# Kernel optimization log

Measured on AMD Instinct MI355X. Metric: run time of the kernel, lower is better.

The kernel has to match this reference:

```python
import jax, jax.numpy as jnp
import numpy as np

DIM = 1024
N_HEADS = 16
HEAD_DIM = DIM // N_HEADS
SCALE = HEAD_DIM ** -0.5


def setup_inputs() -> dict:
    key = jax.random.key(0)
    k1, k2, k3 = jax.random.split(key, 3)
    x = jax.random.normal(k1, (4, 2048, DIM), dtype=jnp.float32)
    w_qkv = jax.random.normal(k2, (DIM, 3 * DIM), dtype=jnp.float32) * (DIM ** -0.5)
    w_proj = jax.random.normal(k3, (DIM, DIM), dtype=jnp.float32) * (DIM ** -0.5)
    b_proj = jnp.zeros((DIM,), dtype=jnp.float32)
    return {"x": x, "w_qkv": w_qkv, "w_proj": w_proj, "b_proj": b_proj}


def reference(x, w_qkv, w_proj, b_proj):
    b, s, d = x.shape
    # qkv projection (no bias), split into q, k, v with per-head layout
    qkv = (x @ w_qkv).reshape(b, s, 3, N_HEADS, HEAD_DIM)
    q, k, v = jnp.moveaxis(qkv, 2, 0)  # each [b, s, h, hd]
    # scaled dot-product attention
    scores = jnp.einsum('bqhd,bkhd->bhqk', q, k) * SCALE
    attn = jax.nn.softmax(scores, axis=-1)
    out = jnp.einsum('bhqk,bkhd->bqhd', attn, v).reshape(b, s, d)
    # output projection (with bias)
    return out @ w_proj + b_proj
```

## Files before the change

kernel.cpp:

```cpp
#include <hip/hip_runtime.h>

#define DIM 1024
#define NHEADS 16
#define HD 64
#define SEQ 2048
#define BATCH 4
#define MROWS (BATCH * SEQ)
#define N3 (3 * DIM)
#define SCALE 0.125f
#define LOG2E 1.4426950408889634f
#define SM_C (SCALE * LOG2E)
#define SMAX 16.0f

typedef __attribute__((ext_vector_type(8))) __bf16 bf16x8;
typedef __attribute__((ext_vector_type(4))) __bf16 bf16x4;
typedef __attribute__((ext_vector_type(4))) float f32x4;

#define MFMA16(a, b, c) __builtin_amdgcn_mfma_f32_16x16x32_bf16((a), (b), (c), 0, 0, 0)

#define GLDS16(g, l)                                                        \
  __builtin_amdgcn_global_load_lds(                                         \
      (const __attribute__((address_space(1))) void*)(g),                   \
      (__attribute__((address_space(3))) void*)(l), 16, 0, 0)

__device__ __forceinline__ unsigned short f2bf(float f) {
  union { float f; unsigned u; } v;
  v.f = f;
  unsigned r = v.u + 0x7fffu + ((v.u >> 16) & 1u);
  return (unsigned short)(r >> 16);
}

__device__ __forceinline__ float exp2_hw(float x) {
  float r;
  asm("v_exp_f32 %0, %1" : "=v"(r) : "v"(x));
  return r;
}


__device__ __forceinline__ void tcast_tile(const float* __restrict__ in,
                                           unsigned short* __restrict__ out,
                                           int K, int N, int bx, int by,
                                           int t) {
  __shared__ float tile[32][33];
  int c = t & 31, r8 = t >> 5;
  int n0 = bx * 32, k0 = by * 32;
#pragma unroll
  for (int i = 0; i < 4; ++i) {
    int kr = r8 + i * 8;
    tile[kr][c] = in[(size_t)(k0 + kr) * N + n0 + c];
  }
  __syncthreads();
#pragma unroll
  for (int i = 0; i < 4; ++i) {
    int nr = r8 + i * 8;
    out[(size_t)(n0 + nr) * K + k0 + c] = f2bf(tile[c][nr]);
  }
}

__global__ void prep_kernel(const float* __restrict__ x,
                            unsigned short* __restrict__ xb,
                            const float* __restrict__ wqkv,
                            unsigned short* __restrict__ wqkvT,
                            const float* __restrict__ wproj,
                            unsigned short* __restrict__ wprojT) {
  const int bid = blockIdx.x, t = threadIdx.x;
  if (bid < 8192) {
    int i = bid * 256 + t;
    float4 v = ((const float4*)x)[i];
    ushort4 o;
    o.x = f2bf(v.x); o.y = f2bf(v.y); o.z = f2bf(v.z); o.w = f2bf(v.w);
    ((ushort4*)xb)[i] = o;
  } else if (bid < 11264) {
    int local = bid - 8192;
    tcast_tile(wqkv, wqkvT, DIM, N3, local % 96, local / 96, t);
  } else {
    int local = bid - 11264;
    tcast_tile(wproj, wprojT, DIM, DIM, local % 32, local / 32, t);
  }
}


__global__ __launch_bounds__(256, 3)
void gemm_qkv_kernel(const unsigned short* __restrict__ A,
                     const unsigned short* __restrict__ Bt,
                     unsigned short* __restrict__ Qb,
                     unsigned short* __restrict__ Kb,
                     unsigned short* __restrict__ Vt) {
  __shared__ __align__(16) unsigned short As[128 * 64];
  __shared__ __align__(16) unsigned short Bs[128 * 64];
  int t = threadIdx.x;
  int w = t >> 6, l = t & 63;
  int lane16 = l & 15, lhi = l >> 4;
  int mbase = blockIdx.y * 128, nbase = blockIdx.x * 128;
  int wm = (w >> 1) * 64, wn = (w & 1) * 64;

  const int srow = t >> 3;
  const int sslot = (t & 7) ^ ((t >> 3) & 7);
  const unsigned short* Ag = A + (size_t)(mbase + srow) * 1024 + sslot * 8;
  const unsigned short* Bg = Bt + (size_t)(nbase + srow) * 1024 + sslot * 8;

  const int sl0 = ((lhi ^ (lane16 & 7)) << 4);
  const char* Ard = (const char*)As + (wm + lane16) * 128;
  const char* Brd = (const char*)Bs + (wn + lane16) * 128;

  f32x4 acc[4][4];
  f32x4 z4 = {0.f, 0.f, 0.f, 0.f};
#pragma unroll
  for (int i = 0; i < 4; ++i)
#pragma unroll
    for (int j = 0; j < 4; ++j) acc[i][j] = z4;

  for (int kt = 0; kt < 1024; kt += 64) {
#pragma unroll
    for (int i = 0; i < 4; ++i) {
      GLDS16(Ag + (size_t)(i * 32) * 1024 + kt, (char*)As + i * 4096 + w * 1024);
      GLDS16(Bg + (size_t)(i * 32) * 1024 + kt, (char*)Bs + i * 4096 + w * 1024);
    }
    __syncthreads();
#pragma unroll
    for (int kh = 0; kh < 2; ++kh) {
      const int so = sl0 ^ (kh << 6);
      bf16x8 af[4], bfr[4];
#pragma unroll
      for (int mi = 0; mi < 4; ++mi)
        af[mi] = *(const bf16x8*)(Ard + mi * 2048 + so);
#pragma unroll
      for (int ni = 0; ni < 4; ++ni)
        bfr[ni] = *(const bf16x8*)(Brd + ni * 2048 + so);
#pragma unroll
      for (int mi = 0; mi < 4; ++mi)
#pragma unroll
        for (int ni = 0; ni < 4; ++ni)
          acc[mi][ni] = MFMA16(af[mi], bfr[ni], acc[mi][ni]);
    }
    __syncthreads();
  }

#pragma unroll
  for (int mi = 0; mi < 4; ++mi) {
#pragma unroll
    for (int ni = 0; ni < 4; ++ni) {
#pragma unroll
      for (int r = 0; r < 4; ++r) {
        int grow = mbase + wm + mi * 16 + (lhi << 2) + r;
        int gcol = nbase + wn + ni * 16 + lane16;
        int b = grow >> 11, s = grow & 2047;
        unsigned short val = f2bf(acc[mi][ni][r]);
        if (gcol < 1024) {
          int h = gcol >> 6, d = gcol & 63;
          Qb[((size_t)(b * 16 + h) * 2048 + s) * 64 + d] = val;
        } else if (gcol < 2048) {
          int n2 = gcol - 1024;
          int h = n2 >> 6, d = n2 & 63;
          Kb[((size_t)(b * 16 + h) * 2048 + s) * 64 + d] = val;
        } else {
          int n2 = gcol - 2048;
          int h = n2 >> 6, d = n2 & 63;
          Vt[((size_t)(b * 16 + h) * 64 + d) * 2048 + s] = val;
        }
      }
    }
  }
}


__global__ __launch_bounds__(512, 4)
void attn_kernel(const unsigned short* __restrict__ Qb,
                 const unsigned short* __restrict__ Kb,
                 const unsigned short* __restrict__ Vt,
                 unsigned short* __restrict__ attn) {
  __shared__ __align__(16) unsigned short Ks[2][4096];
  __shared__ __align__(16) unsigned short Vs[2][4096];
  __shared__ __align__(16) unsigned short Ps[8][32][72];

  const int t = threadIdx.x, wv = t >> 6, l = t & 63;
  const int lane16 = l & 15, lhi = l >> 4;

  const int bid = blockIdx.x;
  const int nid = (bid & 7) * 64 + (bid >> 3);
  const int qg = nid & 7, h = (nid >> 3) & 15, b = nid >> 7;

  const unsigned short* Qp = Qb + (size_t)(b * NHEADS + h) * SEQ * HD;
  const unsigned short* Kp = Kb + (size_t)(b * NHEADS + h) * SEQ * HD;
  const unsigned short* Vp = Vt + (size_t)(b * NHEADS + h) * HD * SEQ;

  const int q0 = qg * 256 + wv * 32;

  bf16x8 qa[2][2];
#pragma unroll
  for (int mi = 0; mi < 2; ++mi)
#pragma unroll
    for (int kh = 0; kh < 2; ++kh)
      qa[mi][kh] = *(const bf16x8*)(Qp + (size_t)(q0 + mi * 16 + lane16) * HD +
                                    kh * 32 + lhi * 8);

  const int srow = t >> 3;
  const unsigned short* kg = Kp + srow * HD + (((t & 7) ^ ((t >> 5) & 7)) * 8);
  const unsigned short* vg =
      Vp + (size_t)srow * SEQ + (((t & 7) ^ ((t >> 3) & 7)) * 8);

  const int key = lane16 & 7;
  const int off0 = (lhi ^ key) << 4;
  const int off1 = off0 ^ 64;
  const char* krd = (const char*)&Ks[0][0] + lane16 * 512;
  const char* vrd = (const char*)&Vs[0][0] + lane16 * 128;
  unsigned short* pwr = &Ps[wv][0][lane16 * 4];
  const unsigned short* prd = &Ps[wv][lane16][lhi * 8];

  f32x4 z4 = {0.f, 0.f, 0.f, 0.f};
  f32x4 o[2][4];
  float lsum[2][4];
#pragma unroll
  for (int mi = 0; mi < 2; ++mi)
#pragma unroll
    for (int nd = 0; nd < 4; ++nd) o[mi][nd] = z4;
#pragma unroll
  for (int mi = 0; mi < 2; ++mi)
#pragma unroll
    for (int r = 0; r < 4; ++r) lsum[mi][r] = 0.f;

  GLDS16(kg, (char*)&Ks[0][0] + wv * 1024);
  GLDS16(vg, (char*)&Vs[0][0] + wv * 1024);
  __syncthreads();

  int cur = 0;
  for (int ti = 0; ti < SEQ / 64; ++ti) {
    if (ti < SEQ / 64 - 1) {
      const int kb = (ti + 1) * 64;
      GLDS16(kg + (size_t)kb * HD, (char*)&Ks[cur ^ 1][0] + wv * 1024);
      GLDS16(vg + kb, (char*)&Vs[cur ^ 1][0] + wv * 1024);
    }

    const char* kp = krd + cur * 8192;
    bf16x8 kf[4][2];
#pragma unroll
    for (int ni = 0; ni < 4; ++ni) {
      kf[ni][0] = *(const bf16x8*)(kp + ni * 128 + off0);
      kf[ni][1] = *(const bf16x8*)(kp + ni * 128 + off1);
    }
#pragma unroll
    for (int mi = 0; mi < 2; ++mi) {
      f32x4 s[4];
      __builtin_amdgcn_s_setprio(1);
#pragma unroll
      for (int ni = 0; ni < 4; ++ni) {
        f32x4 a = MFMA16(qa[mi][0], kf[ni][0], z4);
        s[ni] = MFMA16(qa[mi][1], kf[ni][1], a);
      }
      __builtin_amdgcn_s_setprio(0);
#pragma unroll
      for (int r = 0; r < 4; ++r) {
        float p0 = exp2_hw(__builtin_fmaf(s[0][r], SM_C, -SMAX));
        float p1 = exp2_hw(__builtin_fmaf(s[1][r], SM_C, -SMAX));
        float p2 = exp2_hw(__builtin_fmaf(s[2][r], SM_C, -SMAX));
        float p3 = exp2_hw(__builtin_fmaf(s[3][r], SM_C, -SMAX));
        lsum[mi][r] += (p0 + p1) + (p2 + p3);
        bf16x4 pk;
        pk[0] = (__bf16)p0; pk[1] = (__bf16)p1;
        pk[2] = (__bf16)p2; pk[3] = (__bf16)p3;
        *(bf16x4*)(pwr + (mi * 16 + (lhi << 2) + r) * 72) = pk;
      }
    }

    bf16x8 pa[2][2];
#pragma unroll
    for (int mi = 0; mi < 2; ++mi)
#pragma unroll
      for (int kvh = 0; kvh < 2; ++kvh)
        pa[mi][kvh] = *(const bf16x8*)(prd + mi * 16 * 72 + kvh * 32);
    const char* vp2 = vrd + cur * 8192;
    __builtin_amdgcn_s_setprio(1);
#pragma unroll
    for (int nd = 0; nd < 4; ++nd) {
      bf16x8 v0 = *(const bf16x8*)(vp2 + nd * 2048 + off0);
      bf16x8 v1 = *(const bf16x8*)(vp2 + nd * 2048 + off1);
#pragma unroll
      for (int mi = 0; mi < 2; ++mi) {
        o[mi][nd] = MFMA16(pa[mi][0], v0, o[mi][nd]);
        o[mi][nd] = MFMA16(pa[mi][1], v1, o[mi][nd]);
      }
    }
    __builtin_amdgcn_s_setprio(0);
    __syncthreads();
    cur ^= 1;
  }

#pragma unroll
  for (int mi = 0; mi < 2; ++mi)
#pragma unroll
    for (int r = 0; r < 4; ++r) {
      float ls = lsum[mi][r];
      ls += __shfl_xor(ls, 1);
      ls += __shfl_xor(ls, 2);
      ls += __shfl_xor(ls, 4);
      ls += __shfl_xor(ls, 8);
      lsum[mi][r] = 1.0f / ls;
    }
  size_t orow_base = (size_t)b * SEQ;
#pragma unroll
  for (int mi = 0; mi < 2; ++mi)
#pragma unroll
    for (int nd = 0; nd < 4; ++nd)
#pragma unroll
      for (int r = 0; r < 4; ++r) {
        int row = q0 + mi * 16 + (lhi << 2) + r;
        attn[(orow_base + row) * DIM + h * HD + nd * 16 + lane16] =
            f2bf(o[mi][nd][r] * lsum[mi][r]);
      }
}


__global__ __launch_bounds__(256, 3)
void gemm_proj_kernel(const unsigned short* __restrict__ A,
                      const unsigned short* __restrict__ Bt,
                      const float* __restrict__ bias,
                      float* __restrict__ out) {
  __shared__ __align__(16) unsigned short Asp[128 * 64];
  __shared__ __align__(16) unsigned short Bsp[128 * 64];
  int t = threadIdx.x;
  int w = t >> 6, l = t & 63;
  int lane16 = l & 15, lhi = l >> 4;
  int mbase = blockIdx.y * 128, nbase = blockIdx.x * 128;
  int wm = (w >> 1) * 64, wn = (w & 1) * 64;

  const int srow = t >> 3;
  const int sslot = (t & 7) ^ ((t >> 3) & 7);
  const unsigned short* Ag = A + (size_t)(mbase + srow) * 1024 + sslot * 8;
  const unsigned short* Bg = Bt + (size_t)(nbase + srow) * 1024 + sslot * 8;

  const int sl0 = ((lhi ^ (lane16 & 7)) << 4);
  const char* Ard = (const char*)Asp + (wm + lane16) * 128;
  const char* Brd = (const char*)Bsp + (wn + lane16) * 128;

  f32x4 acc[4][4];
  f32x4 z4 = {0.f, 0.f, 0.f, 0.f};
#pragma unroll
  for (int i = 0; i < 4; ++i)
#pragma unroll
    for (int j = 0; j < 4; ++j) acc[i][j] = z4;

  for (int kt = 0; kt < 1024; kt += 64) {
#pragma unroll
    for (int i = 0; i < 4; ++i) {
      GLDS16(Ag + (size_t)(i * 32) * 1024 + kt, (char*)Asp + i * 4096 + w * 1024);
      GLDS16(Bg + (size_t)(i * 32) * 1024 + kt, (char*)Bsp + i * 4096 + w * 1024);
    }
    __syncthreads();
#pragma unroll
    for (int kh = 0; kh < 2; ++kh) {
      const int so = sl0 ^ (kh << 6);
      bf16x8 af[4], bfr[4];
#pragma unroll
      for (int mi = 0; mi < 4; ++mi)
        af[mi] = *(const bf16x8*)(Ard + mi * 2048 + so);
#pragma unroll
      for (int ni = 0; ni < 4; ++ni)
        bfr[ni] = *(const bf16x8*)(Brd + ni * 2048 + so);
#pragma unroll
      for (int mi = 0; mi < 4; ++mi)
#pragma unroll
        for (int ni = 0; ni < 4; ++ni)
          acc[mi][ni] = MFMA16(af[mi], bfr[ni], acc[mi][ni]);
    }
    __syncthreads();
  }

#pragma unroll
  for (int mi = 0; mi < 4; ++mi) {
#pragma unroll
    for (int ni = 0; ni < 4; ++ni) {
#pragma unroll
      for (int r = 0; r < 4; ++r) {
        int grow = mbase + wm + mi * 16 + (lhi << 2) + r;
        int gcol = nbase + wn + ni * 16 + lane16;
        out[(size_t)grow * 1024 + gcol] = acc[mi][ni][r] + bias[gcol];
      }
    }
  }
}


extern "C" void kernel_launch(void* const* d_in, const int* in_sizes, int n_in,
                              void* d_out, int out_size, void* d_ws,
                              size_t ws_size, hipStream_t stream) {
  const float* x = (const float*)d_in[0];
  const float* w_qkv = (const float*)d_in[1];
  const float* w_proj = (const float*)d_in[2];
  const float* b_proj = (const float*)d_in[3];
  float* out = (float*)d_out;
  char* ws = (char*)d_ws;

  unsigned short* xb = (unsigned short*)(ws);
  unsigned short* attnb = (unsigned short*)(ws);
  unsigned short* wqkvT = (unsigned short*)(ws + (16ull << 20));
  unsigned short* wprojT = (unsigned short*)(ws + (22ull << 20));
  unsigned short* Qb = (unsigned short*)(ws + (24ull << 20));
  unsigned short* Kb = (unsigned short*)(ws + (40ull << 20));
  unsigned short* Vt = (unsigned short*)(ws + (56ull << 20));

  prep_kernel<<<12288, 256, 0, stream>>>(x, xb, w_qkv, wqkvT, w_proj, wprojT);
  gemm_qkv_kernel<<<dim3(N3 / 128, MROWS / 128), 256, 0, stream>>>(xb, wqkvT, Qb, Kb, Vt);
  attn_kernel<<<512, 512, 0, stream>>>(Qb, Kb, Vt, attnb);
  gemm_proj_kernel<<<dim3(DIM / 128, MROWS / 128), 256, 0, stream>>>(attnb, wprojT, b_proj, out);
}
```

Baseline: 206.5 us.

## Load K and V fragments directly from global memory, dropping LDS staging

```diff
diff --git a/kernel.cpp b/kernel.cpp
--- a/kernel.cpp
+++ b/kernel.cpp
@@ -169,8 +169,6 @@
                  const unsigned short* __restrict__ Kb,
                  const unsigned short* __restrict__ Vt,
                  unsigned short* __restrict__ attn) {
-  __shared__ __align__(16) unsigned short Ks[2][4096];
-  __shared__ __align__(16) unsigned short Vs[2][4096];
   __shared__ __align__(16) unsigned short Ps[8][32][72];
 
   const int t = threadIdx.x, wv = t >> 6, l = t & 63;
@@ -194,16 +192,9 @@
       qa[mi][kh] = *(const bf16x8*)(Qp + (size_t)(q0 + mi * 16 + lane16) * HD +
                                     kh * 32 + lhi * 8);
 
-  const int srow = t >> 3;
-  const unsigned short* kg = Kp + srow * HD + (((t & 7) ^ ((t >> 5) & 7)) * 8);
-  const unsigned short* vg =
-      Vp + (size_t)srow * SEQ + (((t & 7) ^ ((t >> 3) & 7)) * 8);
-
-  const int key = lane16 & 7;
-  const int off0 = (lhi ^ key) << 4;
-  const int off1 = off0 ^ 64;
-  const char* krd = (const char*)&Ks[0][0] + lane16 * 512;
-  const char* vrd = (const char*)&Vs[0][0] + lane16 * 128;
+  const unsigned short* kfb = Kp + (size_t)(4 * lane16) * HD + lhi * 8;
+  const unsigned short* vfb = Vp + (size_t)lane16 * SEQ + lhi * 8;
+
   unsigned short* pwr = &Ps[wv][0][lane16 * 4];
   const unsigned short* prd = &Ps[wv][lane16][lhi * 8];
 
@@ -219,35 +210,23 @@
 #pragma unroll
     for (int r = 0; r < 4; ++r) lsum[mi][r] = 0.f;
 
-  GLDS16(kg, (char*)&Ks[0][0] + wv * 1024);
-  GLDS16(vg, (char*)&Vs[0][0] + wv * 1024);
-  __syncthreads();
-
-  int cur = 0;
-  for (int ti = 0; ti < SEQ / 64; ++ti) {
-    if (ti < SEQ / 64 - 1) {
-      const int kb = (ti + 1) * 64;
-      GLDS16(kg + (size_t)kb * HD, (char*)&Ks[cur ^ 1][0] + wv * 1024);
-      GLDS16(vg + kb, (char*)&Vs[cur ^ 1][0] + wv * 1024);
-    }
-
-    const char* kp = krd + cur * 8192;
+  for (int kb = 0; kb < SEQ; kb += 64) {
     bf16x8 kf[4][2];
 #pragma unroll
     for (int ni = 0; ni < 4; ++ni) {
-      kf[ni][0] = *(const bf16x8*)(kp + ni * 128 + off0);
-      kf[ni][1] = *(const bf16x8*)(kp + ni * 128 + off1);
-    }
+      const unsigned short* kr = kfb + (size_t)(kb + ni) * HD;
+      kf[ni][0] = *(const bf16x8*)(kr);
+      kf[ni][1] = *(const bf16x8*)(kr + 32);
+    }
+
 #pragma unroll
     for (int mi = 0; mi < 2; ++mi) {
       f32x4 s[4];
-      __builtin_amdgcn_s_setprio(1);
 #pragma unroll
       for (int ni = 0; ni < 4; ++ni) {
         f32x4 a = MFMA16(qa[mi][0], kf[ni][0], z4);
         s[ni] = MFMA16(qa[mi][1], kf[ni][1], a);
       }
-      __builtin_amdgcn_s_setprio(0);
 #pragma unroll
       for (int r = 0; r < 4; ++r) {
         float p0 = exp2_hw(__builtin_fmaf(s[0][r], SM_C, -SMAX));
@@ -268,21 +247,17 @@
 #pragma unroll
       for (int kvh = 0; kvh < 2; ++kvh)
         pa[mi][kvh] = *(const bf16x8*)(prd + mi * 16 * 72 + kvh * 32);
-    const char* vp2 = vrd + cur * 8192;
-    __builtin_amdgcn_s_setprio(1);
 #pragma unroll
     for (int nd = 0; nd < 4; ++nd) {
-      bf16x8 v0 = *(const bf16x8*)(vp2 + nd * 2048 + off0);
-      bf16x8 v1 = *(const bf16x8*)(vp2 + nd * 2048 + off1);
+      const unsigned short* vr = vfb + (size_t)(nd * 16) * SEQ + kb;
+      bf16x8 v0 = *(const bf16x8*)(vr);
+      bf16x8 v1 = *(const bf16x8*)(vr + 32);
 #pragma unroll
       for (int mi = 0; mi < 2; ++mi) {
         o[mi][nd] = MFMA16(pa[mi][0], v0, o[mi][nd]);
         o[mi][nd] = MFMA16(pa[mi][1], v1, o[mi][nd]);
       }
     }
-    __builtin_amdgcn_s_setprio(0);
-    __syncthreads();
-    cur ^= 1;
   }
 
 #pragma unroll
```

After: 345.0 us. 1.67x slower.
